# Kernel optimization log

Measured on AMD Instinct MI355X. Metric: run time of the kernel, lower is better.

## Reference

```python
import jax, jax.numpy as jnp
import numpy as np

# Dimensions (match init_kwargs / input_specs)
V, B, T, D, E, K = 2, 4, 1024, 512, 16, 4
H = 4 * D  # expert hidden dim


def setup_inputs() -> dict:
    key = jax.random.key(0)
    ks = jax.random.split(key, 8)
    s = 0.02  # weight init scale
    return {
        "view0": jax.random.normal(ks[0], (B, T, D), jnp.float32),
        "view1": jax.random.normal(ks[1], (B, T, D), jnp.float32),
        "proj_w": jax.random.normal(ks[2], (V, D, D), jnp.float32) * s,
        "proj_b": jnp.zeros((V, D), jnp.float32),
        "router_w": jax.random.normal(ks[3], (V, D, D), jnp.float32) * s,
        "expert_keys": jax.random.normal(ks[4], (E, D), jnp.float32),
        "w1": jax.random.normal(ks[5], (E, D, H), jnp.float32) * s,
        "b1": jnp.zeros((E, H), jnp.float32),
        "w2": jax.random.normal(ks[6], (E, H, D), jnp.float32) * s,
        "b2": jnp.zeros((E, D), jnp.float32),
    }


def _laplace_gate(r, keys):
    # r: [B,T,D] routed token, keys: [E,D]. logits = -euclidean distance (torch.cdist p=2).
    d2 = (jnp.sum(r * r, -1, keepdims=True)
          - 2.0 * jnp.einsum('btd,ed->bte', r, keys)
          + jnp.sum(keys * keys, -1))                      # [B,T,E]
    logits = -jnp.sqrt(jnp.maximum(d2, 0.0))
    topv, topi = jax.lax.top_k(logits, K)                  # [B,T,K]
    gate = jax.nn.softmax(topv, axis=-1)                   # exp(v - logsumexp(v))
    # Scatter top-k gates into dense [B,T,E] combine weights (top_k indices are distinct).
    g_dense = jnp.sum(jax.nn.one_hot(topi, E, dtype=r.dtype) * gate[..., None], axis=-2)
    return g_dense


def reference(view0, view1, proj_w, proj_b, router_w, expert_keys, w1, b1, w2, b2):
    fused = jnp.zeros_like(view0)
    for v, x in enumerate((view0, view1)):            # small fixed n_views loop
        h = jnp.einsum('btd,de->bte', x, proj_w[v]) + proj_b[v]          # per-view projection
        g = _laplace_gate(jnp.einsum('btd,de->bte', h, router_w[v]), expert_keys)  # [B,T,E]
        # Dense all-expert compute, then masked combine (same math as per-token dispatch).
        hid = jax.nn.gelu(jnp.einsum('btd,edh->bteh', h, w1) + b1, approximate=False)  # [B,T,E,H]
        out = jnp.einsum('bteh,ehd->bted', hid, w2) + b2                 # [B,T,E,D]
        fused = fused + jnp.einsum('bte,bted->btd', g, out)
    return fused
```

## Files before the change

kernel.cpp:

```cpp
#include <hip/hip_runtime.h>
#include <math.h>

#define BT   4096
#define DIM  512
#define NE   16
#define TOPK 4
#define HID  2048
#define NVIEW 2
#define HSPLIT 2
#define HS   (HID/HSPLIT)

#define BM 128

typedef float f4 __attribute__((ext_vector_type(4)));
typedef float f32x4 __attribute__((ext_vector_type(4)));
typedef short s16x8 __attribute__((ext_vector_type(8)));
typedef unsigned short u16x8 __attribute__((ext_vector_type(8)));
typedef unsigned short u16x4 __attribute__((ext_vector_type(4)));

__device__ __forceinline__ unsigned short f2bf(float f) {
    unsigned u = __float_as_uint(f);
    unsigned r = u + 0x7FFFu + ((u >> 16) & 1u);
    return (unsigned short)(r >> 16);
}
__device__ __forceinline__ float gelu_exact(float x) {
    return 0.5f * x * (1.0f + erff(x * 0.70710678118654752f));
}
__device__ __forceinline__ int swz(int r) { return (r ^ (r >> 3)) & 7; }

__global__ __launch_bounds__(256)
void gemm0_k(const float* __restrict__ A, const float* __restrict__ B,
             const float* __restrict__ bias, float* __restrict__ C,
             unsigned short* __restrict__ bfout)
{
    const int m0 = blockIdx.x * 64, n0 = blockIdx.y * 64;
    __shared__ float As[16][64];
    __shared__ float Bs[16][64];
    const int tid = threadIdx.x;
    const int tx = tid & 15, ty = tid >> 4;
    const int ar = tid >> 2, ak = (tid & 3) * 4;
    const int bk = tid >> 4, bn = (tid & 15) * 4;
    const float* Ar = A + (size_t)(m0 + ar) * DIM;

    float acc[4][4] = {};
    for (int kt = 0; kt < DIM; kt += 16) {
        f4 av = *(const f4*)(Ar + kt + ak);
        f4 bv = *(const f4*)(B + (size_t)(kt + bk) * DIM + n0 + bn);
        __syncthreads();
        As[ak+0][ar] = av[0]; As[ak+1][ar] = av[1];
        As[ak+2][ar] = av[2]; As[ak+3][ar] = av[3];
        *(f4*)&Bs[bk][bn] = bv;
        __syncthreads();
        #pragma unroll
        for (int k = 0; k < 16; ++k) {
            f4 a = *(const f4*)&As[k][ty*4];
            f4 b = *(const f4*)&Bs[k][tx*4];
            #pragma unroll
            for (int i = 0; i < 4; ++i)
                #pragma unroll
                for (int j = 0; j < 4; ++j)
                    acc[i][j] = fmaf(a[i], b[j], acc[i][j]);
        }
    }
    #pragma unroll
    for (int i = 0; i < 4; ++i) {
        int gr = m0 + ty*4 + i;
        f4 v;
        #pragma unroll
        for (int j = 0; j < 4; ++j)
            v[j] = acc[i][j] + (bias ? bias[n0 + tx*4 + j] : 0.f);
        *(f4*)(C + (size_t)gr * DIM + n0 + tx*4) = v;
        if (bfout) {
            u16x4 w = { f2bf(v[0]), f2bf(v[1]), f2bf(v[2]), f2bf(v[3]) };
            *(u16x4*)&bfout[(size_t)gr * DIM + n0 + tx*4] = w;
        }
    }
}

template<int MODE>
__global__ __launch_bounds__(256, 2)
void moe_mfma_k(const unsigned short* __restrict__ Ab,
                const float* __restrict__ Bg,
                const float* __restrict__ biasb,
                void* __restrict__ Cout,
                int Kdim, int lda, int ldb, int ldc, int bias_ld, long strideB,
                const int* __restrict__ offsets, const int* __restrict__ jobs,
                const int* __restrict__ jobCount,
                const int* __restrict__ pair_token, int first)
{
    const int job = blockIdx.x;
    if (job >= *jobCount) return;
    const int e  = jobs[2*job];
    const int m0 = jobs[2*job+1];
    const int rowbase = offsets[e];
    const int nrows   = offsets[e+1] - rowbase;
    const float* Bp    = Bg + (long)e * strideB;
    const float* biasp = biasb + (long)e * bias_ld;
    const int n0 = blockIdx.y * 128;

    __shared__ unsigned short As[128*64];
    __shared__ unsigned short Bs[128*64];

    const int tid = threadIdx.x;

    const unsigned short* arow;
    {
        int r = m0 + (tid & 127);
        if (r >= nrows) r = nrows - 1;
        if (MODE == 1) arow = Ab + (size_t)pair_token[rowbase + r] * lda;
        else           arow = Ab + (size_t)(rowbase + r) * lda;
    }
    const int arr = tid & 127;
    const int acs = (tid >> 7) * 4;

    const int kq0 = tid >> 5;
    const int nq0 = tid & 31;
    const int kq1 = kq0 + 8;

    const int lane = tid & 63;
    const int wid  = tid >> 6;
    const int wm = wid >> 1, wn = wid & 1;
    const int fr = lane & 15, fq = lane >> 4;

    f32x4 acc[4][4] = {};
    u16x8 areg[4];
    f4 breg[2][4];

    #pragma unroll
    for (int c = 0; c < 4; ++c)
        areg[c] = *(const u16x8*)(arow + (acs + c) * 8);
    {
        const float* bs0 = Bp + (size_t)(kq0*4) * ldb + n0 + nq0*4;
        const float* bs1 = Bp + (size_t)(kq1*4) * ldb + n0 + nq0*4;
        #pragma unroll
        for (int j = 0; j < 4; ++j) { breg[0][j] = *(const f4*)(bs0 + j*ldb);
                                      breg[1][j] = *(const f4*)(bs1 + j*ldb); }
    }

    for (int kt = 0; kt < Kdim; kt += 64) {
        __syncthreads();
        #pragma unroll
        for (int c = 0; c < 4; ++c) {
            int ch = acs + c;
            *(u16x8*)&As[arr*64 + ((ch ^ swz(arr)) << 3)] = areg[c];
        }
        #pragma unroll
        for (int cell = 0; cell < 2; ++cell) {
            int kq = cell ? kq1 : kq0;
            #pragma unroll
            for (int j = 0; j < 4; ++j) {
                int n = nq0*4 + j;
                u16x4 w = { f2bf(breg[cell][0][j]), f2bf(breg[cell][1][j]),
                            f2bf(breg[cell][2][j]), f2bf(breg[cell][3][j]) };
                *(u16x4*)&Bs[n*64 + (((kq>>1) ^ swz(n)) << 3) + ((kq&1) << 2)] = w;
            }
        }
        __syncthreads();
        if (kt + 64 < Kdim) {
            #pragma unroll
            for (int c = 0; c < 4; ++c)
                areg[c] = *(const u16x8*)(arow + kt + 64 + (acs + c) * 8);
            const float* bs0 = Bp + (size_t)(kt + 64 + kq0*4) * ldb + n0 + nq0*4;
            const float* bs1 = Bp + (size_t)(kt + 64 + kq1*4) * ldb + n0 + nq0*4;
            #pragma unroll
            for (int j = 0; j < 4; ++j) { breg[0][j] = *(const f4*)(bs0 + j*ldb);
                                          breg[1][j] = *(const f4*)(bs1 + j*ldb); }
        }
        #pragma unroll
        for (int s = 0; s < 2; ++s) {
            s16x8 a[4], b[4];
            const int kc = s*4 + fq;
            #pragma unroll
            for (int m = 0; m < 4; ++m) {
                int row = wm*64 + m*16 + fr;
                a[m] = *(const s16x8*)&As[row*64 + ((kc ^ swz(row)) << 3)];
            }
            #pragma unroll
            for (int n = 0; n < 4; ++n) {
                int col = wn*64 + n*16 + fr;
                b[n] = *(const s16x8*)&Bs[col*64 + ((kc ^ swz(col)) << 3)];
            }
            #pragma unroll
            for (int m = 0; m < 4; ++m)
                #pragma unroll
                for (int n = 0; n < 4; ++n)
                    acc[m][n] = __builtin_amdgcn_mfma_f32_16x16x32_bf16(
                        a[m], b[n], acc[m][n], 0, 0, 0);
        }
    }

    float bv[4];
    #pragma unroll
    for (int n = 0; n < 4; ++n) bv[n] = biasp[n0 + wn*64 + n*16 + fr];
    #pragma unroll
    for (int m = 0; m < 4; ++m) {
        #pragma unroll
        for (int rg = 0; rg < 4; ++rg) {
            int gr = m0 + wm*64 + m*16 + fq*4 + rg;
            if (gr >= nrows) continue;
            size_t rowoff = (size_t)(rowbase + gr) * ldc;
            #pragma unroll
            for (int n = 0; n < 4; ++n) {
                int gc = n0 + wn*64 + n*16 + fr;
                float x = acc[m][n][rg];
                if (MODE == 1) {
                    x = gelu_exact(x + bv[n]);
                    ((unsigned short*)Cout)[rowoff + gc] = f2bf(x);
                } else {
                    float* pc = (float*)Cout + rowoff + gc;
                    x += first ? bv[n] : *pc;
                    *pc = x;
                }
            }
        }
    }
}

__global__ __launch_bounds__(256)
void gate_k(const float* __restrict__ r, const float* __restrict__ keys,
            int* __restrict__ topidx, float* __restrict__ gates)
{
    const int wave = threadIdx.x >> 6;
    const int lane = threadIdx.x & 63;
    const int t = blockIdx.x * 4 + wave;

    float rv[8];
    const float* rrow = r + (long)t * DIM;
    #pragma unroll
    for (int j = 0; j < 8; ++j) rv[j] = rrow[lane + j*64];

    float logit[NE];
    #pragma unroll
    for (int e = 0; e < NE; ++e) {
        const float* krow = keys + e * DIM;
        float s = 0.f;
        #pragma unroll
        for (int j = 0; j < 8; ++j) {
            float d = rv[j] - krow[lane + j*64];
            s = fmaf(d, d, s);
        }
        #pragma unroll
        for (int o = 32; o > 0; o >>= 1) s += __shfl_xor(s, o, 64);
        logit[e] = -sqrtf(fmaxf(s, 0.f));
    }
    int sel[TOPK]; float selv[TOPK];
    unsigned mask = 0;
    #pragma unroll
    for (int k = 0; k < TOPK; ++k) {
        float best = -INFINITY; int bi = 0;
        #pragma unroll
        for (int e = 0; e < NE; ++e) {
            if (mask & (1u << e)) continue;
            if (logit[e] > best) { best = logit[e]; bi = e; }
        }
        mask |= 1u << bi; sel[k] = bi; selv[k] = best;
    }
    float m = selv[0], se = 0.f, ex[TOPK];
    #pragma unroll
    for (int k = 0; k < TOPK; ++k) { ex[k] = expf(selv[k] - m); se += ex[k]; }
    if (lane == 0) {
        #pragma unroll
        for (int k = 0; k < TOPK; ++k) {
            topidx[t*TOPK + k] = sel[k];
            gates [t*TOPK + k] = ex[k] / se;
        }
    }
}

__global__ void count_k(const int* __restrict__ topidx, int base4, int n4,
                        int* __restrict__ counts)
{
    int i = blockIdx.x * blockDim.x + threadIdx.x;
    if (i < n4) atomicAdd(&counts[topidx[base4 + i]], 1);
}

__global__ void scan_jobs_k(const int* __restrict__ counts, int* __restrict__ offsets,
                            int* __restrict__ jobs, int* __restrict__ jobCount)
{
    int off = 0, nj = 0;
    for (int e = 0; e < NE; ++e) {
        offsets[e] = off;
        int n = counts[e];
        for (int m0 = 0; m0 < n; m0 += BM) { jobs[2*nj] = e; jobs[2*nj+1] = m0; ++nj; }
        off += n;
    }
    offsets[NE] = off;
    *jobCount = nj;
}

__global__ void assign_k(const int* __restrict__ topidx, int base4, int baseTok, int n4,
                         const int* __restrict__ offsets, int* __restrict__ cursors,
                         int* __restrict__ pair_token, int* __restrict__ token_slot)
{
    int i = blockIdx.x * blockDim.x + threadIdx.x;
    if (i >= n4) return;
    int tl = i >> 2;
    int e = topidx[base4 + i];
    int slot = offsets[e] + atomicAdd(&cursors[e], 1);
    pair_token[slot] = baseTok + tl;
    token_slot[i] = slot;
}

__global__ __launch_bounds__(128)
void combine_k(const float* __restrict__ pout, const float* __restrict__ gates,
               const int* __restrict__ token_slot, float* __restrict__ out,
               int baseTok, int add)
{
    const int tl = blockIdx.x;
    const int gt = baseTok + tl;
    const int d4 = threadIdx.x;
    float4 acc = add ? ((const float4*)out)[(long)gt*128 + d4]
                     : make_float4(0.f, 0.f, 0.f, 0.f);
    #pragma unroll
    for (int k = 0; k < TOPK; ++k) {
        int slot = token_slot[tl*TOPK + k];
        float g  = gates[(long)gt*TOPK + k];
        float4 p = ((const float4*)pout)[(long)slot*128 + d4];
        acc.x = fmaf(g, p.x, acc.x); acc.y = fmaf(g, p.y, acc.y);
        acc.z = fmaf(g, p.z, acc.z); acc.w = fmaf(g, p.w, acc.w);
    }
    ((float4*)out)[(long)gt*128 + d4] = acc;
}

extern "C" void kernel_launch(void* const* d_in, const int* in_sizes, int n_in,
                              void* d_out, int out_size, void* d_ws, size_t ws_size,
                              hipStream_t stream)
{
    const float* view[2]  = {(const float*)d_in[0], (const float*)d_in[1]};
    const float* proj_w   = (const float*)d_in[2];
    const float* proj_b   = (const float*)d_in[3];
    const float* router_w = (const float*)d_in[4];
    const float* keys     = (const float*)d_in[5];
    const float* w1       = (const float*)d_in[6];
    const float* b1       = (const float*)d_in[7];
    const float* w2       = (const float*)d_in[8];
    const float* b2       = (const float*)d_in[9];
    float* out = (float*)d_out;

    const size_t hF  = (size_t)BT * DIM;
    const size_t hbF = hF / 2;
    const size_t metaF = (size_t)BT * TOPK;
    const size_t metaI = (size_t)BT * TOPK * 3 + 16 + 16 + 1 + (NE + 1) + 320;
    int C = 512;
    {
        const int cand[3] = {2048, 1024, 512};
        for (int ci = 0; ci < 3; ++ci) {
            size_t needF = hF + hbF + 2 * (size_t)2048 * cand[ci] + metaF + metaI;
            if (needF * 4 + (4u << 20) <= ws_size) { C = cand[ci]; break; }
        }
    }
    const int chunks = BT / C;
    const int mj = C / 32 + NE;

    float* h32 = (float*)d_ws;
    unsigned short* hb = (unsigned short*)(h32 + hF);
    float* chunkA = h32 + hF + hbF;
    float* chunkB = chunkA + (size_t)2048 * C;
    float* gates  = chunkB + (size_t)2048 * C;
    int* topidx     = (int*)(gates + metaF);
    int* token_slot = topidx + BT*TOPK;
    int* pair_token = token_slot + BT*TOPK;
    int* counts     = pair_token + BT*TOPK;
    int* cursors    = counts + NE;
    int* jobCount   = cursors + NE;
    int* offsets    = jobCount + 1;
    int* jobs       = offsets + NE + 1;

    float* r = chunkA;

    const long sB1 = (long)DIM * HID;
    const long sB2 = (long)HID * DIM;

    for (int v = 0; v < NVIEW; ++v) {
        dim3 g0(BT/64, DIM/64);
        gemm0_k<<<g0, 256, 0, stream>>>(view[v], proj_w + (long)v*DIM*DIM,
                                        proj_b + v*DIM, h32, hb);
        gemm0_k<<<g0, 256, 0, stream>>>(h32, router_w + (long)v*DIM*DIM,
                                        nullptr, r, nullptr);
        gate_k<<<BT/4, 256, 0, stream>>>(r, keys, topidx, gates);

        for (int c = 0; c < chunks; ++c) {
            const int base4 = c * C * TOPK, baseTok = c * C, n4 = C * TOPK;
            (void)hipMemsetAsync(counts, 0, 33 * sizeof(int), stream);
            count_k<<<(n4 + 255)/256, 256, 0, stream>>>(topidx, base4, n4, counts);
            scan_jobs_k<<<1, 1, 0, stream>>>(counts, offsets, jobs, jobCount);
            assign_k<<<(n4 + 255)/256, 256, 0, stream>>>(topidx, base4, baseTok, n4,
                                                         offsets, cursors,
                                                         pair_token, token_slot);
            for (int s = 0; s < HSPLIT; ++s) {
                moe_mfma_k<1><<<dim3(mj, HS/128), 256, 0, stream>>>(
                    hb, w1 + s*HS, b1 + s*HS, (void*)chunkA,
                    DIM, DIM, HID, HS, HID, sB1,
                    offsets, jobs, jobCount, pair_token, 0);
                moe_mfma_k<2><<<dim3(mj, DIM/128), 256, 0, stream>>>(
                    (const unsigned short*)chunkA, w2 + (long)s*HS*DIM, b2,
                    (void*)chunkB,
                    HS, HS, DIM, DIM, DIM, sB2,
                    offsets, jobs, jobCount, nullptr, (s == 0) ? 1 : 0);
            }
            combine_k<<<C, 128, 0, stream>>>(chunkB, gates, token_slot, out,
                                             baseTok, v);
        }
    }
}
```

Measured before the change: 1.256 ms.

## Pre-transpose expert weights to bf16 and double-buffer MoE GEMM with direct LDS loads

```diff
diff --git a/kernel.cpp b/kernel.cpp
--- a/kernel.cpp
+++ b/kernel.cpp
@@ -7,10 +7,9 @@
 #define TOPK 4
 #define HID  2048
 #define NVIEW 2
-#define HSPLIT 2
+#define HSPLIT 4
 #define HS   (HID/HSPLIT)
-
-#define BM 128
+#define BMJ  128
 
 typedef float f4 __attribute__((ext_vector_type(4)));
 typedef float f32x4 __attribute__((ext_vector_type(4)));
@@ -27,6 +26,12 @@
     return 0.5f * x * (1.0f + erff(x * 0.70710678118654752f));
 }
 __device__ __forceinline__ int swz(int r) { return (r ^ (r >> 3)) & 7; }
+
+__device__ __forceinline__ void gload16(const void* g, void* l) {
+    __builtin_amdgcn_global_load_lds(
+        (const __attribute__((address_space(1))) unsigned int*)g,
+        (__attribute__((address_space(3))) unsigned int*)l, 16, 0, 0);
+}
 
 __global__ __launch_bounds__(256)
 void gemm0_k(const float* __restrict__ A, const float* __restrict__ B,
@@ -77,16 +82,48 @@
     }
 }
 
+__global__ __launch_bounds__(256)
+void transpcast_k(const float* __restrict__ in, long e_stride, int ld_in,
+                  unsigned short* __restrict__ outp)
+{
+    __shared__ float t[64][65];
+    const int e = blockIdx.x;
+    const int k0 = blockIdx.y * 64, n0 = blockIdx.z * 64;
+    const float* src = in + (size_t)e * e_stride + (size_t)k0 * ld_in + n0;
+    const int tid = threadIdx.x;
+    {
+        int rr = tid >> 4, c4 = (tid & 15) * 4;
+        #pragma unroll
+        for (int j = 0; j < 4; ++j) {
+            f4 v = *(const f4*)(src + (size_t)(rr + j*16) * ld_in + c4);
+            t[rr + j*16][c4+0] = v[0]; t[rr + j*16][c4+1] = v[1];
+            t[rr + j*16][c4+2] = v[2]; t[rr + j*16][c4+3] = v[3];
+        }
+    }
+    __syncthreads();
+    {
+        int rn = tid >> 3, k8 = (tid & 7) * 8;
+        unsigned short* dst = outp + (size_t)e * (512*512);
+        #pragma unroll
+        for (int j = 0; j < 2; ++j) {
+            int n = rn + j*32;
+            u16x8 w;
+            #pragma unroll
+            for (int i2 = 0; i2 < 8; ++i2) w[i2] = f2bf(t[k8 + i2][n]);
+            *(u16x8*)(dst + (size_t)(n0 + n)*512 + k0 + k8) = w;
+        }
+    }
+}
+
 template<int MODE>
 __global__ __launch_bounds__(256, 2)
-void moe_mfma_k(const unsigned short* __restrict__ Ab,
-                const float* __restrict__ Bg,
-                const float* __restrict__ biasb,
-                void* __restrict__ Cout,
-                int Kdim, int lda, int ldb, int ldc, int bias_ld, long strideB,
-                const int* __restrict__ offsets, const int* __restrict__ jobs,
-                const int* __restrict__ jobCount,
-                const int* __restrict__ pair_token, int first)
+void moe_k(const unsigned short* __restrict__ Ab,
+           const unsigned short* __restrict__ Bt,
+           const float* __restrict__ biasb, void* __restrict__ Cout,
+           int bias_ld,
+           const int* __restrict__ offsets, const int* __restrict__ jobs,
+           const int* __restrict__ jobCount, const int* __restrict__ pair_token,
+           int first)
 {
     const int job = blockIdx.x;
     if (job >= *jobCount) return;
@@ -94,91 +131,57 @@
     const int m0 = jobs[2*job+1];
     const int rowbase = offsets[e];
     const int nrows   = offsets[e+1] - rowbase;
-    const float* Bp    = Bg + (long)e * strideB;
-    const float* biasp = biasb + (long)e * bias_ld;
     const int n0 = blockIdx.y * 128;
-
-    __shared__ unsigned short As[128*64];
-    __shared__ unsigned short Bs[128*64];
-
-    const int tid = threadIdx.x;
-
-    const unsigned short* arow;
-    {
-        int r = m0 + (tid & 127);
-        if (r >= nrows) r = nrows - 1;
-        if (MODE == 1) arow = Ab + (size_t)pair_token[rowbase + r] * lda;
-        else           arow = Ab + (size_t)(rowbase + r) * lda;
-    }
-    const int arr = tid & 127;
-    const int acs = (tid >> 7) * 4;
-
-    const int kq0 = tid >> 5;
-    const int nq0 = tid & 31;
-    const int kq1 = kq0 + 8;
-
-    const int lane = tid & 63;
-    const int wid  = tid >> 6;
+    const unsigned short* Bte = Bt + (size_t)e * (512*512);
+
+    __shared__ unsigned short lds[4*128*64];
+    unsigned short* As0 = lds;
+    unsigned short* Bs0 = lds + 8192;
+    unsigned short* As1 = lds + 16384;
+    unsigned short* Bs1 = lds + 24576;
+
+    const int tid  = threadIdx.x;
+    const int wid  = tid >> 6, lane = tid & 63;
+    const int sub  = lane >> 3, cc = lane & 7;
     const int wm = wid >> 1, wn = wid & 1;
     const int fr = lane & 15, fq = lane >> 4;
 
+    size_t aoff[4], boff[4];
+    #pragma unroll
+    for (int i = 0; i < 4; ++i) {
+        int r = wid*32 + i*8 + sub;
+        int gr = m0 + r; if (gr >= nrows) gr = nrows - 1;
+        size_t arow = (MODE == 1) ? (size_t)pair_token[rowbase + gr]
+                                  : (size_t)(rowbase + gr);
+        aoff[i] = arow * 512 + (size_t)((cc ^ swz(r)) << 3);
+        boff[i] = (size_t)(n0 + r) * 512 + (size_t)((cc ^ swz(r)) << 3);
+    }
+
     f32x4 acc[4][4] = {};
-    u16x8 areg[4];
-    f4 breg[2][4];
-
-    #pragma unroll
-    for (int c = 0; c < 4; ++c)
-        areg[c] = *(const u16x8*)(arow + (acs + c) * 8);
-    {
-        const float* bs0 = Bp + (size_t)(kq0*4) * ldb + n0 + nq0*4;
-        const float* bs1 = Bp + (size_t)(kq1*4) * ldb + n0 + nq0*4;
-        #pragma unroll
-        for (int j = 0; j < 4; ++j) { breg[0][j] = *(const f4*)(bs0 + j*ldb);
-                                      breg[1][j] = *(const f4*)(bs1 + j*ldb); }
-    }
-
-    for (int kt = 0; kt < Kdim; kt += 64) {
-        __syncthreads();
-        #pragma unroll
-        for (int c = 0; c < 4; ++c) {
-            int ch = acs + c;
-            *(u16x8*)&As[arr*64 + ((ch ^ swz(arr)) << 3)] = areg[c];
-        }
-        #pragma unroll
-        for (int cell = 0; cell < 2; ++cell) {
-            int kq = cell ? kq1 : kq0;
-            #pragma unroll
-            for (int j = 0; j < 4; ++j) {
-                int n = nq0*4 + j;
-                u16x4 w = { f2bf(breg[cell][0][j]), f2bf(breg[cell][1][j]),
-                            f2bf(breg[cell][2][j]), f2bf(breg[cell][3][j]) };
-                *(u16x4*)&Bs[n*64 + (((kq>>1) ^ swz(n)) << 3) + ((kq&1) << 2)] = w;
-            }
-        }
-        __syncthreads();
-        if (kt + 64 < Kdim) {
-            #pragma unroll
-            for (int c = 0; c < 4; ++c)
-                areg[c] = *(const u16x8*)(arow + kt + 64 + (acs + c) * 8);
-            const float* bs0 = Bp + (size_t)(kt + 64 + kq0*4) * ldb + n0 + nq0*4;
-            const float* bs1 = Bp + (size_t)(kt + 64 + kq1*4) * ldb + n0 + nq0*4;
-            #pragma unroll
-            for (int j = 0; j < 4; ++j) { breg[0][j] = *(const f4*)(bs0 + j*ldb);
-                                          breg[1][j] = *(const f4*)(bs1 + j*ldb); }
-        }
-        #pragma unroll
-        for (int s = 0; s < 2; ++s) {
+
+    auto stage = [&](int kt, unsigned short* Aw, unsigned short* Bw) {
+        #pragma unroll
+        for (int i = 0; i < 4; ++i) {
+            gload16((const char*)Ab  + ((aoff[i] + kt) << 1),
+                    (char*)Aw + ((wid*4 + i) << 10));
+            gload16((const char*)Bte + ((boff[i] + kt) << 1),
+                    (char*)Bw + ((wid*4 + i) << 10));
+        }
+    };
+    auto compute = [&](const unsigned short* Ar, const unsigned short* Br) {
+        #pragma unroll
+        for (int s2 = 0; s2 < 2; ++s2) {
+            const int kc = s2*4 + fq;
             s16x8 a[4], b[4];
-            const int kc = s*4 + fq;
             #pragma unroll
             for (int m = 0; m < 4; ++m) {
                 int row = wm*64 + m*16 + fr;
-                a[m] = *(const s16x8*)&As[row*64 + ((kc ^ swz(row)) << 3)];
+                a[m] = *(const s16x8*)&Ar[row*64 + ((kc ^ swz(row)) << 3)];
             }
             #pragma unroll
             for (int n = 0; n < 4; ++n) {
                 int col = wn*64 + n*16 + fr;
-                b[n] = *(const s16x8*)&Bs[col*64 + ((kc ^ swz(col)) << 3)];
+                b[n] = *(const s16x8*)&Br[col*64 + ((kc ^ swz(col)) << 3)];
             }
             #pragma unroll
             for (int m = 0; m < 4; ++m)
@@ -187,18 +190,30 @@
                     acc[m][n] = __builtin_amdgcn_mfma_f32_16x16x32_bf16(
                         a[m], b[n], acc[m][n], 0, 0, 0);
         }
+    };
+
+    stage(0, As0, Bs0);
+    #pragma unroll 1
+    for (int it = 0; it < 8; it += 2) {
+        __syncthreads();
+        if (it + 1 < 8) stage((it+1)*64, As1, Bs1);
+        compute(As0, Bs0);
+        __syncthreads();
+        if (it + 2 < 8) stage((it+2)*64, As0, Bs0);
+        compute(As1, Bs1);
     }
 
     float bv[4];
     #pragma unroll
-    for (int n = 0; n < 4; ++n) bv[n] = biasp[n0 + wn*64 + n*16 + fr];
-    #pragma unroll
-    for (int m = 0; m < 4; ++m) {
+    for (int n = 0; n < 4; ++n)
+        bv[n] = biasb[(size_t)e * bias_ld + n0 + wn*64 + n*16 + fr];
+    #pragma unroll
+    for (int m = 0; m < 4; ++m)
         #pragma unroll
         for (int rg = 0; rg < 4; ++rg) {
             int gr = m0 + wm*64 + m*16 + fq*4 + rg;
             if (gr >= nrows) continue;
-            size_t rowoff = (size_t)(rowbase + gr) * ldc;
+            size_t rowoff = (size_t)(rowbase + gr) * 512;
             #pragma unroll
             for (int n = 0; n < 4; ++n) {
                 int gc = n0 + wn*64 + n*16 + fr;
@@ -208,12 +223,10 @@
                     ((unsigned short*)Cout)[rowoff + gc] = f2bf(x);
                 } else {
                     float* pc = (float*)Cout + rowoff + gc;
-                    x += first ? bv[n] : *pc;
-                    *pc = x;
+                    *pc = x + (first ? bv[n] : *pc);
                 }
             }
         }
-    }
 }
 
 __global__ __launch_bounds__(256)
@@ -267,38 +280,42 @@
     }
 }
 
-__global__ void count_k(const int* __restrict__ topidx, int base4, int n4,
-                        int* __restrict__ counts)
-{
-    int i = blockIdx.x * blockDim.x + threadIdx.x;
-    if (i < n4) atomicAdd(&counts[topidx[base4 + i]], 1);
-}
-
-__global__ void scan_jobs_k(const int* __restrict__ counts, int* __restrict__ offsets,
-                            int* __restrict__ jobs, int* __restrict__ jobCount)
-{
-    int off = 0, nj = 0;
-    for (int e = 0; e < NE; ++e) {
-        offsets[e] = off;
-        int n = counts[e];
-        for (int m0 = 0; m0 < n; m0 += BM) { jobs[2*nj] = e; jobs[2*nj+1] = m0; ++nj; }
-        off += n;
-    }
-    offsets[NE] = off;
-    *jobCount = nj;
-}
-
-__global__ void assign_k(const int* __restrict__ topidx, int base4, int baseTok, int n4,
-                         const int* __restrict__ offsets, int* __restrict__ cursors,
-                         int* __restrict__ pair_token, int* __restrict__ token_slot)
-{
-    int i = blockIdx.x * blockDim.x + threadIdx.x;
-    if (i >= n4) return;
-    int tl = i >> 2;
-    int e = topidx[base4 + i];
-    int slot = offsets[e] + atomicAdd(&cursors[e], 1);
-    pair_token[slot] = baseTok + tl;
-    token_slot[i] = slot;
+__global__ __launch_bounds__(256)
+void route_k(const int* __restrict__ topidx, int C,
+             int* __restrict__ offsets4, int* __restrict__ jobs4,
+             int* __restrict__ jobCount4,
+             int* __restrict__ pair_token, int* __restrict__ token_slot, int mj)
+{
+    const int chunk = blockIdx.x;
+    const int n4 = C * TOPK, base4 = chunk * n4, baseTok = chunk * C;
+    __shared__ int cnt[NE], cur[NE], off[NE+1];
+    const int tid = threadIdx.x;
+    if (tid < NE) { cnt[tid] = 0; cur[tid] = 0; }
+    __syncthreads();
+    for (int i = tid; i < n4; i += 256) atomicAdd(&cnt[topidx[base4 + i]], 1);
+    __syncthreads();
+    if (tid == 0) {
+        int o = 0, nj = 0;
+        int* jb = jobs4 + chunk * 2 * mj;
+        for (int e = 0; e < NE; ++e) {
+            off[e] = o;
+            offsets4[chunk*(NE+1) + e] = o;
+            for (int m0 = 0; m0 < cnt[e]; m0 += BMJ) {
+                jb[2*nj] = e; jb[2*nj+1] = m0; ++nj;
+            }
+            o += cnt[e];
+        }
+        off[NE] = o;
+        offsets4[chunk*(NE+1) + NE] = o;
+        jobCount4[chunk] = nj;
+    }
+    __syncthreads();
+    for (int i = tid; i < n4; i += 256) {
+        int et = topidx[base4 + i];
+        int slot = off[et] + atomicAdd(&cur[et], 1);
+        pair_token[base4 + slot] = baseTok + (i >> 2);
+        token_slot[base4 + i] = slot;
+    }
 }
 
 __global__ __launch_bounds__(128)
@@ -337,69 +354,65 @@
     const float* b2       = (const float*)d_in[9];
     float* out = (float*)d_out;
 
-    const size_t hF  = (size_t)BT * DIM;
-    const size_t hbF = hF / 2;
-    const size_t metaF = (size_t)BT * TOPK;
-    const size_t metaI = (size_t)BT * TOPK * 3 + 16 + 16 + 1 + (NE + 1) + 320;
-    int C = 512;
+    const size_t MB = 1u << 20;
+    int C = 1024;
     {
-        const int cand[3] = {2048, 1024, 512};
+        const int cand[3] = {4096, 2048, 1024};
         for (int ci = 0; ci < 3; ++ci) {
-            size_t needF = hF + hbF + 2 * (size_t)2048 * cand[ci] + metaF + metaI;
-            if (needF * 4 + (4u << 20) <= ws_size) { C = cand[ci]; break; }
+            size_t cA = (size_t)cand[ci] * TOPK * HS * 2;
+            size_t cB = (size_t)cand[ci] * TOPK * DIM * 4;
+            size_t need = 16*MB + 4*MB + cA + cB + 512*1024;
+            if (need + 1*MB <= ws_size) { C = cand[ci]; break; }
         }
     }
     const int chunks = BT / C;
-    const int mj = C / 32 + NE;
-
-    float* h32 = (float*)d_ws;
-    unsigned short* hb = (unsigned short*)(h32 + hF);
-    float* chunkA = h32 + hF + hbF;
-    float* chunkB = chunkA + (size_t)2048 * C;
-    float* gates  = chunkB + (size_t)2048 * C;
-    int* topidx     = (int*)(gates + metaF);
+    const int mj = C/32 + NE;
+
+    char* base = (char*)d_ws;
+    unsigned short* w1Ts = (unsigned short*)base;
+    unsigned short* w2Ts = (unsigned short*)(base + 8*MB);
+    float* h32 = (float*)base;
+    unsigned short* hb = (unsigned short*)(base + 16*MB);
+    unsigned short* chunkA = (unsigned short*)(base + 20*MB);
+    const size_t cAB = (size_t)C * TOPK * HS * 2;
+    float* chunkB = (float*)(base + 20*MB + cAB);
+    float* gates  = (float*)((char*)chunkB + (size_t)C * TOPK * DIM * 4);
+    int* topidx     = (int*)(gates + (size_t)BT*TOPK);
     int* token_slot = topidx + BT*TOPK;
     int* pair_token = token_slot + BT*TOPK;
-    int* counts     = pair_token + BT*TOPK;
-    int* cursors    = counts + NE;
-    int* jobCount   = cursors + NE;
-    int* offsets    = jobCount + 1;
-    int* jobs       = offsets + NE + 1;
-
-    float* r = chunkA;
-
-    const long sB1 = (long)DIM * HID;
-    const long sB2 = (long)HID * DIM;
+    int* offsets4   = pair_token + BT*TOPK;
+    int* jobCount4  = offsets4 + 4*(NE+1);
+    int* jobs4      = jobCount4 + 4;
+    float* r = (float*)chunkA;
 
     for (int v = 0; v < NVIEW; ++v) {
         dim3 g0(BT/64, DIM/64);
-        gemm0_k<<<g0, 256, 0, stream>>>(view[v], proj_w + (long)v*DIM*DIM,
+        gemm0_k<<<g0, 256, 0, stream>>>(view[v], proj_w + (size_t)v*DIM*DIM,
                                         proj_b + v*DIM, h32, hb);
-        gemm0_k<<<g0, 256, 0, stream>>>(h32, router_w + (long)v*DIM*DIM,
+        gemm0_k<<<g0, 256, 0, stream>>>(h32, router_w + (size_t)v*DIM*DIM,
                                         nullptr, r, nullptr);
         gate_k<<<BT/4, 256, 0, stream>>>(r, keys, topidx, gates);
-
+        route_k<<<chunks, 256, 0, stream>>>(topidx, C, offsets4, jobs4,
+                                            jobCount4, pair_token, token_slot, mj);
         for (int c = 0; c < chunks; ++c) {
-            const int base4 = c * C * TOPK, baseTok = c * C, n4 = C * TOPK;
-            (void)hipMemsetAsync(counts, 0, 33 * sizeof(int), stream);
-            count_k<<<(n4 + 255)/256, 256, 0, stream>>>(topidx, base4, n4, counts);
-            scan_jobs_k<<<1, 1, 0, stream>>>(counts, offsets, jobs, jobCount);
-            assign_k<<<(n4 + 255)/256, 256, 0, stream>>>(topidx, base4, baseTok, n4,
-                                                         offsets, cursors,
-                                                         pair_token, token_slot);
+            const int b4 = c * C * TOPK;
+            const int* off_c = offsets4 + c*(NE+1);
+            const int* jb_c  = jobs4 + c*2*mj;
+            const int* jc_c  = jobCount4 + c;
             for (int s = 0; s < HSPLIT; ++s) {
-                moe_mfma_k<1><<<dim3(mj, HS/128), 256, 0, stream>>>(
-                    hb, w1 + s*HS, b1 + s*HS, (void*)chunkA,
-                    DIM, DIM, HID, HS, HID, sB1,
-                    offsets, jobs, jobCount, pair_token, 0);
-                moe_mfma_k<2><<<dim3(mj, DIM/128), 256, 0, stream>>>(
-                    (const unsigned short*)chunkA, w2 + (long)s*HS*DIM, b2,
-                    (void*)chunkB,
-                    HS, HS, DIM, DIM, DIM, sB2,
-                    offsets, jobs, jobCount, nullptr, (s == 0) ? 1 : 0);
+                transpcast_k<<<dim3(NE,8,8), 256, 0, stream>>>(
+                    w1 + (size_t)s*HS, (long)DIM*HID, HID, w1Ts);
+                transpcast_k<<<dim3(NE,8,8), 256, 0, stream>>>(
+                    w2 + (size_t)s*HS*DIM, (long)HID*DIM, DIM, w2Ts);
+                moe_k<1><<<dim3(mj,4), 256, 0, stream>>>(
+                    hb, w1Ts, b1 + s*HS, (void*)chunkA, HID,
+                    off_c, jb_c, jc_c, pair_token + b4, 0);
+                moe_k<2><<<dim3(mj,4), 256, 0, stream>>>(
+                    chunkA, w2Ts, b2, (void*)chunkB, DIM,
+                    off_c, jb_c, jc_c, nullptr, (s == 0) ? 1 : 0);
             }
-            combine_k<<<C, 128, 0, stream>>>(chunkB, gates, token_slot, out,
-                                             baseTok, v);
-        }
-    }
-}
+            combine_k<<<C, 128, 0, stream>>>(chunkB, gates, token_slot + b4,
+                                             out, c*C, v);
+        }
+    }
+}
```

Result: faster. 1.103 ms (-12.2%).
